# Optimization experiments

Hardware: AMD Instinct MI355X
Metric: run time of the kernel (lower is better)

## Reference

```python
import jax, jax.numpy as jnp
import numpy as np

N = 100_000    # nodes
E = 3_200_000  # distance-labeled multi-hop edges (self-loops excluded upstream)
F = 128        # num_features
H = 128        # hidden (emb_sizes all 128)
C = 40         # num_classes
K = 5          # max_distance
BN_EPS = 1e-5
GIN_EPS = 0.0  # eps=0, learnable_eps=False


def _bn(h, g, b):
    # BatchNorm1d in training mode: biased batch stats over the node axis
    m = h.mean(axis=0)
    v = jnp.mean((h - m) ** 2, axis=0)
    return g * (h - m) * jax.lax.rsqrt(v + BN_EPS) + b


def _spn_layer(h, src, dst, dist, hc, Wa, ba, ga, bta, Wb, bb, gb, btb):
    # SPN layer: softmax per-hop weights, weighted sum aggregation over
    # distance-labeled edges, GIN-style combine, 2-layer MLP (Linear+BN+ReLU).
    w = jax.nn.softmax(hc)                 # [K]
    msg = w[dist][:, None] * h[src]        # [E, H]
    agg = jax.ops.segment_sum(msg, dst, num_segments=N)  # [N, H]
    z = (1.0 + GIN_EPS) * h + agg
    z = jax.nn.relu(_bn(z @ Wa + ba, ga, bta))
    z = jax.nn.relu(_bn(z @ Wb + bb, gb, btb))
    return z


def setup_inputs() -> dict:
    key = jax.random.key(0)
    ks = jax.random.split(key, 16)
    def w(i, shape, s):
        return jax.random.normal(ks[i], shape, dtype=jnp.float32) * s
    sF = 1.0 / np.sqrt(F)
    sH = 1.0 / np.sqrt(H)
    z = lambda n: jnp.zeros((n,), jnp.float32)
    o = lambda n: jnp.ones((n,), jnp.float32)
    return {
        "x": jax.random.normal(ks[0], (N, F), dtype=jnp.float32),
        "edge_index": jax.random.randint(ks[1], (2, E), 0, N, dtype=jnp.int32),
        "edge_dist": jax.random.randint(ks[2], (E,), 0, K, dtype=jnp.int32),  # hop idx = distance-1
        "Wi": w(3, (F, H), sF), "bi": z(H), "gi": o(H), "bti": z(H),
        "hc0": w(4, (K,), 1.0),
        "W0a": w(5, (H, H), sH), "b0a": z(H), "g0a": o(H), "bt0a": z(H),
        "W0b": w(6, (H, H), sH), "b0b": z(H), "g0b": o(H), "bt0b": z(H),
        "hc1": w(7, (K,), 1.0),
        "W1a": w(8, (H, H), sH), "b1a": z(H), "g1a": o(H), "bt1a": z(H),
        "W1b": w(9, (H, H), sH), "b1b": z(H), "g1b": o(H), "bt1b": z(H),
        "Wp1": w(10, (H, H), sH), "bp1": z(H), "gp1": o(H), "btp1": z(H),
        "Wp2": w(11, (H, C), sH), "bp2": z(C),
    }


def reference(x, edge_index, edge_dist, Wi, bi, gi, bti,
              hc0, W0a, b0a, g0a, bt0a, W0b, b0b, g0b, bt0b,
              hc1, W1a, b1a, g1a, bt1a, W1b, b1b, g1b, bt1b,
              Wp1, bp1, gp1, btp1, Wp2, bp2):
    src, dst = edge_index[0], edge_index[1]
    # initial MLP (size=1, final_activation=True)
    h = jax.nn.relu(_bn(x @ Wi + bi, gi, bti))
    # two SPN message-passing layers (dropout is identity at inference)
    h = _spn_layer(h, src, dst, edge_dist, hc0, W0a, b0a, g0a, bt0a, W0b, b0b, g0b, bt0b)
    h = _spn_layer(h, src, dst, edge_dist, hc1, W1a, b1a, g1a, bt1a, W1b, b1b, g1b, bt1b)
    # prediction head (size=2, final_activation=False)
    h = jax.nn.relu(_bn(h @ Wp1 + bp1, gp1, btp1))
    return h @ Wp2 + bp2
```

## Files before the change

kernel.cpp:

```cpp
#include <hip/hip_runtime.h>

#define NN 100000
#define EE 3200000
#define HH 128
#define CC 40
#define KK 5
#define NBUK 391
#define CH 8192
#define CH2 16384

typedef __attribute__((ext_vector_type(8))) short bf16x8;
typedef __attribute__((ext_vector_type(4))) float f32x4;

__device__ inline float b2f(unsigned short u) {
    union { unsigned int i; float f; } c;
    c.i = ((unsigned int)u) << 16;
    return c.f;
}
__device__ inline float b2f_lo(unsigned int u) {
    union { unsigned int i; float f; } c;
    c.i = u << 16;
    return c.f;
}
__device__ inline float b2f_hi(unsigned int u) {
    union { unsigned int i; float f; } c;
    c.i = u & 0xFFFF0000u;
    return c.f;
}
__device__ inline unsigned short f2b(float f) {
    union { float f; unsigned int i; } c;
    c.f = f;
    unsigned int r = c.i + 0x7FFFu + ((c.i >> 16) & 1u);
    return (unsigned short)(r >> 16);
}

__global__ __launch_bounds__(512) void bucket_hist_kernel(const int* __restrict__ dst,
                                                          int* __restrict__ bdeg) {
    __shared__ int h[512];
    int t = threadIdx.x;
    h[t] = 0;
    __syncthreads();
    int base = blockIdx.x * CH2;
    int end = base + CH2;
    if (end > EE) end = EE;
    for (int e = base + t; e < end; e += 512) atomicAdd(&h[dst[e] >> 8], 1);
    __syncthreads();
    int v = h[t];
    if (v > 0) atomicAdd(&bdeg[t], v);
}

__global__ void bucket_scan_kernel(const int* __restrict__ bdeg, int* __restrict__ bbase,
                                   int* __restrict__ gcur, int* __restrict__ offsets,
                                   const float* __restrict__ hc0, const float* __restrict__ hc1,
                                   float* __restrict__ wsm) {
    __shared__ int sh[512];
    int t = threadIdx.x;
    int v = (t < NBUK) ? bdeg[t] : 0;
    sh[t] = v;
    __syncthreads();
    for (int off = 1; off < 512; off <<= 1) {
        int x = (t >= off) ? sh[t - off] : 0;
        __syncthreads();
        sh[t] += x;
        __syncthreads();
    }
    if (t < NBUK) {
        int b = sh[t] - v;
        bbase[t] = b;
        gcur[t] = b;
    }
    if (t == 0) {
        bbase[NBUK] = EE;
        offsets[NN] = EE;
        for (int which = 0; which < 2; ++which) {
            const float* hc = which ? hc1 : hc0;
            float mx = hc[0];
            for (int k = 1; k < KK; ++k) mx = fmaxf(mx, hc[k]);
            float ex0 = expf(hc[0] - mx), ex1 = expf(hc[1] - mx), ex2 = expf(hc[2] - mx);
            float ex3 = expf(hc[3] - mx), ex4 = expf(hc[4] - mx);
            float inv = 1.0f / (ex0 + ex1 + ex2 + ex3 + ex4);
            wsm[which * 8 + 0] = ex0 * inv;
            wsm[which * 8 + 1] = ex1 * inv;
            wsm[which * 8 + 2] = ex2 * inv;
            wsm[which * 8 + 3] = ex3 * inv;
            wsm[which * 8 + 4] = ex4 * inv;
        }
    }
}

__global__ __launch_bounds__(512) void coarse_scatter_kernel(const int* __restrict__ src,
                                                             const int* __restrict__ dst,
                                                             const int* __restrict__ dist,
                                                             int* __restrict__ gcur,
                                                             int* __restrict__ coarse) {
    __shared__ int cnt[512];
    __shared__ int scn[512];
    __shared__ int lofs[512];
    __shared__ int gb[512];
    __shared__ int staging[CH];
    __shared__ int tgt[CH];
    int t = threadIdx.x;
    int base = blockIdx.x * CH;

    cnt[t] = 0;
    __syncthreads();

    int val[16], bb[16];
#pragma unroll
    for (int jj = 0; jj < 16; ++jj) {
        int e = base + jj * 512 + t;
        if (e < EE) {
            int d = dst[e];
            int b = d >> 8;
            bb[jj] = b;
            val[jj] = src[e] | (dist[e] << 17) | ((d & 255) << 20);
            atomicAdd(&cnt[b], 1);
        } else {
            bb[jj] = -1;
            val[jj] = 0;
        }
    }
    __syncthreads();

    int c = cnt[t];
    scn[t] = c;
    __syncthreads();
    for (int off = 1; off < 512; off <<= 1) {
        int x = (t >= off) ? scn[t - off] : 0;
        __syncthreads();
        scn[t] += x;
        __syncthreads();
    }
    lofs[t] = scn[t] - c;
    if (t < NBUK && c > 0) gb[t] = atomicAdd(&gcur[t], c);
    cnt[t] = 0;
    __syncthreads();

#pragma unroll
    for (int jj = 0; jj < 16; ++jj) {
        int b = bb[jj];
        if (b >= 0) {
            int pos = atomicAdd(&cnt[b], 1);
            int slot = lofs[b] + pos;
            staging[slot] = val[jj];
            tgt[slot] = gb[b] + pos;
        }
    }
    __syncthreads();

    int total = scn[511];
    for (int j = t; j < total; j += 512) coarse[tgt[j]] = staging[j];
}

__global__ __launch_bounds__(512) void fine_scatter_kernel(const int* __restrict__ coarse,
                                                           const int* __restrict__ bbase,
                                                           int* __restrict__ offsets,
                                                           int* __restrict__ sorted) {
    __shared__ int cnt[256];
    __shared__ int scn[256];
    __shared__ int cur[256];
    int b = blockIdx.x;
    int t = threadIdx.x;
    if (t < 256) cnt[t] = 0;
    __syncthreads();
    int sb = bbase[b], se = bbase[b + 1];
    for (int idx = sb + t; idx < se; idx += 512)
        atomicAdd(&cnt[(coarse[idx] >> 20) & 255], 1);
    __syncthreads();
    int c = (t < 256) ? cnt[t] : 0;
    if (t < 256) scn[t] = c;
    __syncthreads();
    for (int off = 1; off < 256; off <<= 1) {
        int x = 0;
        if (t < 256 && t >= off) x = scn[t - off];
        __syncthreads();
        if (t < 256) scn[t] += x;
        __syncthreads();
    }
    if (t < 256) {
        int pos = sb + scn[t] - c;
        int node = (b << 8) + t;
        if (node < NN) offsets[node] = pos;
        cur[t] = pos;
    }
    __syncthreads();
    for (int idx = sb + t; idx < se; idx += 512) {
        int v = coarse[idx];
        int p = atomicAdd(&cur[(v >> 20) & 255], 1);
        sorted[p] = (v & 0x1FFFF) | (((v >> 17) & 7) << 20);
    }
}


__global__ __launch_bounds__(256) void convert_x_kernel(const float* __restrict__ x,
                                                        unsigned short* __restrict__ xb) {
    size_t i = (size_t)(blockIdx.x * 256 + threadIdx.x) * 4;
    float4 v = *(const float4*)(x + i);
    ushort4 o;
    o.x = f2b(v.x);
    o.y = f2b(v.y);
    o.z = f2b(v.z);
    o.w = f2b(v.w);
    *(ushort4*)(xb + i) = o;
}

__global__ __launch_bounds__(256) void prep_w_kernel(const float* W0, const float* W1,
                                                     const float* W2, const float* W3,
                                                     const float* W4, const float* W5,
                                                     const float* W6,
                                                     unsigned short* __restrict__ dst) {
    int idx = blockIdx.x * 256 + threadIdx.x;
    if (idx >= 7 * 16384) return;
    int wi = idx / 16384, r = idx - wi * 16384;
    int n = r & 127, k = r >> 7;
    const float* W = wi == 0 ? W0 : wi == 1 ? W1 : wi == 2 ? W2 : wi == 3 ? W3
                   : wi == 4 ? W4 : wi == 5 ? W5 : W6;
    int ncol = (wi == 6) ? CC : 128;
    float v = (n < ncol) ? W[k * ncol + n] : 0.f;
    dst[wi * 16384 + n * 128 + k] = f2b(v);
}


template <int NT, bool TRANSFORM, bool STATS, bool OUTF32>
__global__ __launch_bounds__(256) void mfma_gemm(const unsigned short* __restrict__ Zin,
                                                 const unsigned short* __restrict__ Wt,
                                                 const float* __restrict__ bias, int ncol_real,
                                                 const float* __restrict__ ab,
                                                 void* __restrict__ Uout,
                                                 float* __restrict__ stats) {
    __shared__ unsigned short Zs[128 * 128];
    __shared__ unsigned short Ws[NT * 16 * 128];
    int t = threadIdx.x;
    int m0 = blockIdx.x * 128;
    int c8 = t & 15;

    float av[8], dv[8];
    if constexpr (TRANSFORM) {
#pragma unroll
        for (int j = 0; j < 8; ++j) {
            av[j] = ab[c8 * 8 + j];
            dv[j] = ab[128 + c8 * 8 + j];
        }
    }
#pragma unroll
    for (int it = 0; it < 8; ++it) {
        int chunk = it * 256 + t;
        int r = chunk >> 4;
        int gr = m0 + r;
        bf16x8 v = {};
        if (gr < NN) v = *(const bf16x8*)(Zin + (size_t)gr * 128 + c8 * 8);
        if constexpr (TRANSFORM) {
#pragma unroll
            for (int j = 0; j < 8; ++j) {
                float f = fmaxf(0.f, fmaf(av[j], b2f((unsigned short)v[j]), dv[j]));
                v[j] = (short)f2b(f);
            }
        }
        int ks = c8 * 8;
        *(bf16x8*)(&Zs[r * 128 + (ks ^ ((r & 7) << 3))]) = v;
    }
    for (int chunk = t; chunk < NT * 16 * 16; chunk += 256) {
        int r = chunk >> 4, cc = chunk & 15;
        bf16x8 v = *(const bf16x8*)(Wt + r * 128 + cc * 8);
        int ks = cc * 8;
        *(bf16x8*)(&Ws[r * 128 + (ks ^ ((r & 7) << 3))]) = v;
    }
    __syncthreads();

    int l = t & 63, w = t >> 6;
    int lr = l & 15, lg = l >> 4;

    f32x4 acc[2][NT];
#pragma unroll
    for (int mt = 0; mt < 2; ++mt)
#pragma unroll
        for (int nt = 0; nt < NT; ++nt) acc[mt][nt] = (f32x4){0.f, 0.f, 0.f, 0.f};

#pragma unroll
    for (int kc = 0; kc < 4; ++kc) {
        int ks = kc * 32 + lg * 8;
        bf16x8 afr[2];
#pragma unroll
        for (int mt = 0; mt < 2; ++mt) {
            int row = w * 32 + mt * 16 + lr;
            afr[mt] = *(const bf16x8*)(&Zs[row * 128 + (ks ^ ((row & 7) << 3))]);
        }
#pragma unroll
        for (int nt = 0; nt < NT; ++nt) {
            int n = nt * 16 + lr;
            bf16x8 bfr = *(const bf16x8*)(&Ws[n * 128 + (ks ^ ((n & 7) << 3))]);
            acc[0][nt] = __builtin_amdgcn_mfma_f32_16x16x32_bf16(afr[0], bfr, acc[0][nt], 0, 0, 0);
            acc[1][nt] = __builtin_amdgcn_mfma_f32_16x16x32_bf16(afr[1], bfr, acc[1][nt], 0, 0, 0);
        }
    }

    float bv[NT];
#pragma unroll
    for (int nt = 0; nt < NT; ++nt) {
        int col = nt * 16 + lr;
        bv[nt] = (col < ncol_real) ? bias[col] : 0.f;
    }
    float s1[NT], s2[NT];
    if constexpr (STATS) {
#pragma unroll
        for (int nt = 0; nt < NT; ++nt) { s1[nt] = 0.f; s2[nt] = 0.f; }
    }

#pragma unroll
    for (int mt = 0; mt < 2; ++mt) {
#pragma unroll
        for (int j = 0; j < 4; ++j) {
            int row = m0 + w * 32 + mt * 16 + lg * 4 + j;
            bool rv = row < NN;
#pragma unroll
            for (int nt = 0; nt < NT; ++nt) {
                float val = acc[mt][nt][j] + bv[nt];
                int col = nt * 16 + lr;
                if constexpr (STATS) {
                    if (rv) { s1[nt] += val; s2[nt] += val * val; }
                }
                if (rv && col < ncol_real) {
                    if constexpr (OUTF32)
                        ((float*)Uout)[(size_t)row * ncol_real + col] = val;
                    else
                        ((unsigned short*)Uout)[(size_t)row * 128 + col] = f2b(val);
                }
            }
        }
    }

    if constexpr (STATS) {
        float* slot = stats + (blockIdx.x & 31) * 256;
#pragma unroll
        for (int nt = 0; nt < NT; ++nt) {
            float a = s1[nt], b = s2[nt];
            a += __shfl_xor(a, 16, 64);
            b += __shfl_xor(b, 16, 64);
            a += __shfl_xor(a, 32, 64);
            b += __shfl_xor(b, 32, 64);
            if (lg == 0) {
                atomicAdd(slot + nt * 16 + lr, a);
                atomicAdd(slot + 128 + nt * 16 + lr, b);
            }
        }
    }
}

__global__ void bn_finalize_kernel(const float* __restrict__ stats, const float* __restrict__ g,
                                   const float* __restrict__ beta, float* __restrict__ ab) {
    int ci = threadIdx.x;
    float s = 0.f, s2 = 0.f;
    for (int k = 0; k < 32; ++k) {
        s += stats[k * 256 + ci];
        s2 += stats[k * 256 + 128 + ci];
    }
    float m = s * (1.0f / NN);
    float var = s2 * (1.0f / NN) - m * m;
    float a = g[ci] * rsqrtf(var + 1e-5f);
    ab[ci] = a;
    ab[128 + ci] = beta[ci] - a * m;
}

__global__ __launch_bounds__(128) void agg_kernel(const unsigned short* __restrict__ U,
                                                  const int* __restrict__ offsets,
                                                  const int* __restrict__ sorted,
                                                  const float* __restrict__ ab,
                                                  const float* __restrict__ wsm,
                                                  unsigned short* __restrict__ Z) {
    __shared__ int ebuf[128];
    __shared__ float wl[8];
    __shared__ f32x4 red[4][32];
    int i = blockIdx.x;
    int t = threadIdx.x;
    int grp = t >> 5;
    int sl = t & 31;
    if (t < KK) wl[t] = wsm[t];

    float a0 = ab[sl * 4 + 0], a1 = ab[sl * 4 + 1], a2 = ab[sl * 4 + 2], a3 = ab[sl * 4 + 3];
    float d0 = ab[128 + sl * 4 + 0], d1 = ab[128 + sl * 4 + 1];
    float d2 = ab[128 + sl * 4 + 2], d3 = ab[128 + sl * 4 + 3];

    int beg = offsets[i], end = offsets[i + 1];
    float acc0 = 0.f, acc1 = 0.f, acc2 = 0.f, acc3 = 0.f;

    for (int base = beg; base < end; base += 128) {
        int n = end - base;
        if (n > 128) n = 128;
        __syncthreads();
        if (t < n) ebuf[t] = sorted[base + t];
        __syncthreads();
        int nfull = n & ~31;
        for (int j0 = grp * 8; j0 < nfull; j0 += 32) {
            uint2 uu[8];
            float ww[8];
#pragma unroll
            for (int k = 0; k < 8; ++k) {
                int e = ebuf[j0 + k];
                ww[k] = wl[e >> 20];
                uu[k] = *(const uint2*)((const char*)U +
                                        ((unsigned int)(e & 0xFFFFF) << 8) + (sl << 3));
            }
#pragma unroll
            for (int k = 0; k < 8; ++k) {
                acc0 = fmaf(ww[k], fmaxf(0.f, fmaf(a0, b2f_lo(uu[k].x), d0)), acc0);
                acc1 = fmaf(ww[k], fmaxf(0.f, fmaf(a1, b2f_hi(uu[k].x), d1)), acc1);
                acc2 = fmaf(ww[k], fmaxf(0.f, fmaf(a2, b2f_lo(uu[k].y), d2)), acc2);
                acc3 = fmaf(ww[k], fmaxf(0.f, fmaf(a3, b2f_hi(uu[k].y), d3)), acc3);
            }
        }
        for (int j = nfull + grp; j < n; j += 4) {
            int e = ebuf[j];
            unsigned int sidx = (unsigned int)(e & 0xFFFFF);
            float w = wl[e >> 20];
            uint2 u = *(const uint2*)((const char*)U + (sidx << 8) + (sl << 3));
            acc0 = fmaf(w, fmaxf(0.f, fmaf(a0, b2f_lo(u.x), d0)), acc0);
            acc1 = fmaf(w, fmaxf(0.f, fmaf(a1, b2f_hi(u.x), d1)), acc1);
            acc2 = fmaf(w, fmaxf(0.f, fmaf(a2, b2f_lo(u.y), d2)), acc2);
            acc3 = fmaf(w, fmaxf(0.f, fmaf(a3, b2f_hi(u.y), d3)), acc3);
        }
    }
    red[grp][sl] = (f32x4){acc0, acc1, acc2, acc3};
    __syncthreads();

    if (t < 64) {
        const float* rf = (const float*)red;
        int c0 = t * 2, c1 = t * 2 + 1;
        float s0 = rf[c0] + rf[128 + c0] + rf[256 + c0] + rf[384 + c0];
        float s1 = rf[c1] + rf[128 + c1] + rf[256 + c1] + rf[384 + c1];
        unsigned int ui = *(const unsigned int*)((const char*)U + ((unsigned int)i << 8) + (t << 2));
        float sa0 = ab[c0], sa1 = ab[c1], sd0 = ab[128 + c0], sd1 = ab[128 + c1];
        s0 += fmaxf(0.f, fmaf(sa0, b2f_lo(ui), sd0));
        s1 += fmaxf(0.f, fmaf(sa1, b2f_hi(ui), sd1));
        unsigned int o = (unsigned int)f2b(s0) | ((unsigned int)f2b(s1) << 16);
        *(unsigned int*)((char*)Z + ((unsigned int)i << 8) + (t << 2)) = o;
    }
}


extern "C" void kernel_launch(void* const* d_in, const int* in_sizes, int n_in,
                              void* d_out, int out_size, void* d_ws, size_t ws_size,
                              hipStream_t stream) {
    const float* x = (const float*)d_in[0];
    const int* ei = (const int*)d_in[1];
    const int* ed = (const int*)d_in[2];
    const float* Wi = (const float*)d_in[3];
    const float* bi = (const float*)d_in[4];
    const float* gi = (const float*)d_in[5];
    const float* bti = (const float*)d_in[6];
    const float* hc0 = (const float*)d_in[7];
    const float* W0a = (const float*)d_in[8];
    const float* b0a = (const float*)d_in[9];
    const float* g0a = (const float*)d_in[10];
    const float* bt0a = (const float*)d_in[11];
    const float* W0b = (const float*)d_in[12];
    const float* b0b = (const float*)d_in[13];
    const float* g0b = (const float*)d_in[14];
    const float* bt0b = (const float*)d_in[15];
    const float* hc1 = (const float*)d_in[16];
    const float* W1a = (const float*)d_in[17];
    const float* b1a = (const float*)d_in[18];
    const float* g1a = (const float*)d_in[19];
    const float* bt1a = (const float*)d_in[20];
    const float* W1b = (const float*)d_in[21];
    const float* b1b = (const float*)d_in[22];
    const float* g1b = (const float*)d_in[23];
    const float* bt1b = (const float*)d_in[24];
    const float* Wp1 = (const float*)d_in[25];
    const float* bp1 = (const float*)d_in[26];
    const float* gp1 = (const float*)d_in[27];
    const float* btp1 = (const float*)d_in[28];
    const float* Wp2 = (const float*)d_in[29];
    const float* bp2 = (const float*)d_in[30];
    float* out = (float*)d_out;

    const int* srcv = ei;
    const int* dstv = ei + EE;

    unsigned short* bufX = (unsigned short*)d_ws;
    unsigned short* bufA = bufX + (size_t)NN * HH;
    unsigned short* bufB = bufA + (size_t)NN * HH;
    unsigned short* wt = bufB + (size_t)NN * HH;
    int* sorted = (int*)(wt + 7 * 16384);
    int* coarse = sorted + EE;
    int* offsets = coarse + EE;
    float* stats = (float*)(offsets + NN + 4);
    float* bnab = stats + 6 * 32 * 256;
    float* wsm = bnab + 6 * 256;
    int* gcur = (int*)(wsm + 16);
    int* bdeg = gcur + 512;
    int* bbase = bdeg + 512;

    hipMemsetAsync(stats, 0, (size_t)(6 * 32 * 256) * sizeof(float), stream);
    hipMemsetAsync(bdeg, 0, 512 * sizeof(int), stream);

    bucket_hist_kernel<<<(EE + CH2 - 1) / CH2, 512, 0, stream>>>(dstv, bdeg);
    bucket_scan_kernel<<<1, 512, 0, stream>>>(bdeg, bbase, gcur, offsets, hc0, hc1, wsm);
    coarse_scatter_kernel<<<(EE + CH - 1) / CH, 512, 0, stream>>>(srcv, dstv, ed, gcur, coarse);
    fine_scatter_kernel<<<NBUK, 512, 0, stream>>>(coarse, bbase, offsets, sorted);

    convert_x_kernel<<<(NN * HH / 4 + 255) / 256, 256, 0, stream>>>(x, bufX);
    prep_w_kernel<<<(7 * 16384 + 255) / 256, 256, 0, stream>>>(Wi, W0a, W0b, W1a, W1b, Wp1, Wp2, wt);

    int gg = (NN + 127) / 128;

    mfma_gemm<8, false, true, false><<<gg, 256, 0, stream>>>(bufX, wt, bi, 128, nullptr, bufA, stats);
    bn_finalize_kernel<<<1, 128, 0, stream>>>(stats, gi, bti, bnab);

    agg_kernel<<<NN, 128, 0, stream>>>(bufA, offsets, sorted, bnab, wsm, bufB);
    mfma_gemm<8, false, true, false><<<gg, 256, 0, stream>>>(bufB, wt + 16384, b0a, 128, nullptr,
                                                             bufA, stats + 8192);
    bn_finalize_kernel<<<1, 128, 0, stream>>>(stats + 8192, g0a, bt0a, bnab + 256);
    mfma_gemm<8, true, true, false><<<gg, 256, 0, stream>>>(bufA, wt + 2 * 16384, b0b, 128,
                                                            bnab + 256, bufB, stats + 2 * 8192);
    bn_finalize_kernel<<<1, 128, 0, stream>>>(stats + 2 * 8192, g0b, bt0b, bnab + 512);

    agg_kernel<<<NN, 128, 0, stream>>>(bufB, offsets, sorted, bnab + 512, wsm + 8, bufA);
    mfma_gemm<8, false, true, false><<<gg, 256, 0, stream>>>(bufA, wt + 3 * 16384, b1a, 128,
                                                             nullptr, bufB, stats + 3 * 8192);
    bn_finalize_kernel<<<1, 128, 0, stream>>>(stats + 3 * 8192, g1a, bt1a, bnab + 768);
    mfma_gemm<8, true, true, false><<<gg, 256, 0, stream>>>(bufB, wt + 4 * 16384, b1b, 128,
                                                            bnab + 768, bufA, stats + 4 * 8192);
    bn_finalize_kernel<<<1, 128, 0, stream>>>(stats + 4 * 8192, g1b, bt1b, bnab + 1024);

    mfma_gemm<8, true, true, false><<<gg, 256, 0, stream>>>(bufA, wt + 5 * 16384, bp1, 128,
                                                            bnab + 1024, bufB, stats + 5 * 8192);
    bn_finalize_kernel<<<1, 128, 0, stream>>>(stats + 5 * 8192, gp1, btp1, bnab + 1280);
    mfma_gemm<3, true, false, true><<<gg, 256, 0, stream>>>(bufB, wt + 6 * 16384, bp2, CC,
                                                            bnab + 1280, out, nullptr);

    (void)in_sizes; (void)n_in; (void)out_size; (void)ws_size;
}
```

Measured before the change: 572.1 us.

## Fuse x fp32-to-bf16 conversion into first GEMM and widen aggregation loads

Removes the separate convert_x kernel: the first GEMM now reads the fp32 input directly and converts it to bf16 while staging it in shared memory. The aggregation kernel is restructured so each edge row is gathered by 16 lanes using 16-byte loads (8 edge slots per block instead of 4), with an 8-way shared-memory reduction. The two memsets are merged into one larger memset. This trades fewer kernel launches and less intermediate traffic for more registers per lane in the gather and a larger reduction buffer.

```diff
diff --git a/kernel.cpp b/kernel.cpp
--- a/kernel.cpp
+++ b/kernel.cpp
@@ -192,18 +192,6 @@
 }
 
 
-__global__ __launch_bounds__(256) void convert_x_kernel(const float* __restrict__ x,
-                                                        unsigned short* __restrict__ xb) {
-    size_t i = (size_t)(blockIdx.x * 256 + threadIdx.x) * 4;
-    float4 v = *(const float4*)(x + i);
-    ushort4 o;
-    o.x = f2b(v.x);
-    o.y = f2b(v.y);
-    o.z = f2b(v.z);
-    o.w = f2b(v.w);
-    *(ushort4*)(xb + i) = o;
-}
-
 __global__ __launch_bounds__(256) void prep_w_kernel(const float* W0, const float* W1,
                                                      const float* W2, const float* W3,
                                                      const float* W4, const float* W5,
@@ -221,8 +209,8 @@
 }
 
 
-template <int NT, bool TRANSFORM, bool STATS, bool OUTF32>
-__global__ __launch_bounds__(256) void mfma_gemm(const unsigned short* __restrict__ Zin,
+template <int NT, bool TRANSFORM, bool STATS, bool OUTF32, bool CVTIN>
+__global__ __launch_bounds__(256) void mfma_gemm(const void* __restrict__ ZinV,
                                                  const unsigned short* __restrict__ Wt,
                                                  const float* __restrict__ bias, int ncol_real,
                                                  const float* __restrict__ ab,
@@ -248,12 +236,25 @@
         int r = chunk >> 4;
         int gr = m0 + r;
         bf16x8 v = {};
-        if (gr < NN) v = *(const bf16x8*)(Zin + (size_t)gr * 128 + c8 * 8);
-        if constexpr (TRANSFORM) {
-#pragma unroll
-            for (int j = 0; j < 8; ++j) {
-                float f = fmaxf(0.f, fmaf(av[j], b2f((unsigned short)v[j]), dv[j]));
-                v[j] = (short)f2b(f);
+        if constexpr (CVTIN) {
+            const float* Zf = (const float*)ZinV;
+            if (gr < NN) {
+                float4 f0 = *(const float4*)(Zf + (size_t)gr * 128 + c8 * 8);
+                float4 f1 = *(const float4*)(Zf + (size_t)gr * 128 + c8 * 8 + 4);
+                v[0] = (short)f2b(f0.x); v[1] = (short)f2b(f0.y);
+                v[2] = (short)f2b(f0.z); v[3] = (short)f2b(f0.w);
+                v[4] = (short)f2b(f1.x); v[5] = (short)f2b(f1.y);
+                v[6] = (short)f2b(f1.z); v[7] = (short)f2b(f1.w);
+            }
+        } else {
+            const unsigned short* Zin = (const unsigned short*)ZinV;
+            if (gr < NN) v = *(const bf16x8*)(Zin + (size_t)gr * 128 + c8 * 8);
+            if constexpr (TRANSFORM) {
+#pragma unroll
+                for (int j = 0; j < 8; ++j) {
+                    float f = fmaxf(0.f, fmaf(av[j], b2f((unsigned short)v[j]), dv[j]));
+                    v[j] = (short)f2b(f);
+                }
             }
         }
         int ks = c8 * 8;
@@ -369,19 +370,22 @@
                                                   unsigned short* __restrict__ Z) {
     __shared__ int ebuf[128];
     __shared__ float wl[8];
-    __shared__ f32x4 red[4][32];
+    __shared__ float red[8][128];
     int i = blockIdx.x;
     int t = threadIdx.x;
-    int grp = t >> 5;
-    int sl = t & 31;
+    int slot = t >> 4;
+    int sl = t & 15;
     if (t < KK) wl[t] = wsm[t];
 
-    float a0 = ab[sl * 4 + 0], a1 = ab[sl * 4 + 1], a2 = ab[sl * 4 + 2], a3 = ab[sl * 4 + 3];
-    float d0 = ab[128 + sl * 4 + 0], d1 = ab[128 + sl * 4 + 1];
-    float d2 = ab[128 + sl * 4 + 2], d3 = ab[128 + sl * 4 + 3];
+    float av[8], dv[8];
+#pragma unroll
+    for (int j = 0; j < 8; ++j) {
+        av[j] = ab[sl * 8 + j];
+        dv[j] = ab[128 + sl * 8 + j];
+    }
 
     int beg = offsets[i], end = offsets[i + 1];
-    float acc0 = 0.f, acc1 = 0.f, acc2 = 0.f, acc3 = 0.f;
+    float acc[8] = {};
 
     for (int base = beg; base < end; base += 128) {
         int n = end - base;
@@ -390,49 +394,56 @@
         if (t < n) ebuf[t] = sorted[base + t];
         __syncthreads();
         int nfull = n & ~31;
-        for (int j0 = grp * 8; j0 < nfull; j0 += 32) {
-            uint2 uu[8];
-            float ww[8];
-#pragma unroll
-            for (int k = 0; k < 8; ++k) {
+        for (int j0 = slot * 4; j0 < nfull; j0 += 32) {
+            uint4 uu[4];
+            float ww[4];
+#pragma unroll
+            for (int k = 0; k < 4; ++k) {
                 int e = ebuf[j0 + k];
                 ww[k] = wl[e >> 20];
-                uu[k] = *(const uint2*)((const char*)U +
-                                        ((unsigned int)(e & 0xFFFFF) << 8) + (sl << 3));
+                uu[k] = *(const uint4*)((const char*)U +
+                                        ((unsigned int)(e & 0xFFFFF) << 8) + (sl << 4));
             }
 #pragma unroll
-            for (int k = 0; k < 8; ++k) {
-                acc0 = fmaf(ww[k], fmaxf(0.f, fmaf(a0, b2f_lo(uu[k].x), d0)), acc0);
-                acc1 = fmaf(ww[k], fmaxf(0.f, fmaf(a1, b2f_hi(uu[k].x), d1)), acc1);
-                acc2 = fmaf(ww[k], fmaxf(0.f, fmaf(a2, b2f_lo(uu[k].y), d2)), acc2);
-                acc3 = fmaf(ww[k], fmaxf(0.f, fmaf(a3, b2f_hi(uu[k].y), d3)), acc3);
+            for (int k = 0; k < 4; ++k) {
+                acc[0] = fmaf(ww[k], fmaxf(0.f, fmaf(av[0], b2f_lo(uu[k].x), dv[0])), acc[0]);
+                acc[1] = fmaf(ww[k], fmaxf(0.f, fmaf(av[1], b2f_hi(uu[k].x), dv[1])), acc[1]);
+                acc[2] = fmaf(ww[k], fmaxf(0.f, fmaf(av[2], b2f_lo(uu[k].y), dv[2])), acc[2]);
+                acc[3] = fmaf(ww[k], fmaxf(0.f, fmaf(av[3], b2f_hi(uu[k].y), dv[3])), acc[3]);
+                acc[4] = fmaf(ww[k], fmaxf(0.f, fmaf(av[4], b2f_lo(uu[k].z), dv[4])), acc[4]);
+                acc[5] = fmaf(ww[k], fmaxf(0.f, fmaf(av[5], b2f_hi(uu[k].z), dv[5])), acc[5]);
+                acc[6] = fmaf(ww[k], fmaxf(0.f, fmaf(av[6], b2f_lo(uu[k].w), dv[6])), acc[6]);
+                acc[7] = fmaf(ww[k], fmaxf(0.f, fmaf(av[7], b2f_hi(uu[k].w), dv[7])), acc[7]);
             }
         }
-        for (int j = nfull + grp; j < n; j += 4) {
+        for (int j = nfull + slot; j < n; j += 8) {
             int e = ebuf[j];
-            unsigned int sidx = (unsigned int)(e & 0xFFFFF);
             float w = wl[e >> 20];
-            uint2 u = *(const uint2*)((const char*)U + (sidx << 8) + (sl << 3));
-            acc0 = fmaf(w, fmaxf(0.f, fmaf(a0, b2f_lo(u.x), d0)), acc0);
-            acc1 = fmaf(w, fmaxf(0.f, fmaf(a1, b2f_hi(u.x), d1)), acc1);
-            acc2 = fmaf(w, fmaxf(0.f, fmaf(a2, b2f_lo(u.y), d2)), acc2);
-            acc3 = fmaf(w, fmaxf(0.f, fmaf(a3, b2f_hi(u.y), d3)), acc3);
-        }
-    }
-    red[grp][sl] = (f32x4){acc0, acc1, acc2, acc3};
-    __syncthreads();
-
-    if (t < 64) {
-        const float* rf = (const float*)red;
-        int c0 = t * 2, c1 = t * 2 + 1;
-        float s0 = rf[c0] + rf[128 + c0] + rf[256 + c0] + rf[384 + c0];
-        float s1 = rf[c1] + rf[128 + c1] + rf[256 + c1] + rf[384 + c1];
-        unsigned int ui = *(const unsigned int*)((const char*)U + ((unsigned int)i << 8) + (t << 2));
-        float sa0 = ab[c0], sa1 = ab[c1], sd0 = ab[128 + c0], sd1 = ab[128 + c1];
-        s0 += fmaxf(0.f, fmaf(sa0, b2f_lo(ui), sd0));
-        s1 += fmaxf(0.f, fmaf(sa1, b2f_hi(ui), sd1));
-        unsigned int o = (unsigned int)f2b(s0) | ((unsigned int)f2b(s1) << 16);
-        *(unsigned int*)((char*)Z + ((unsigned int)i << 8) + (t << 2)) = o;
+            uint4 u = *(const uint4*)((const char*)U +
+                                      ((unsigned int)(e & 0xFFFFF) << 8) + (sl << 4));
+            acc[0] = fmaf(w, fmaxf(0.f, fmaf(av[0], b2f_lo(u.x), dv[0])), acc[0]);
+            acc[1] = fmaf(w, fmaxf(0.f, fmaf(av[1], b2f_hi(u.x), dv[1])), acc[1]);
+            acc[2] = fmaf(w, fmaxf(0.f, fmaf(av[2], b2f_lo(u.y), dv[2])), acc[2]);
+            acc[3] = fmaf(w, fmaxf(0.f, fmaf(av[3], b2f_hi(u.y), dv[3])), acc[3]);
+            acc[4] = fmaf(w, fmaxf(0.f, fmaf(av[4], b2f_lo(u.z), dv[4])), acc[4]);
+            acc[5] = fmaf(w, fmaxf(0.f, fmaf(av[5], b2f_hi(u.z), dv[5])), acc[5]);
+            acc[6] = fmaf(w, fmaxf(0.f, fmaf(av[6], b2f_lo(u.w), dv[6])), acc[6]);
+            acc[7] = fmaf(w, fmaxf(0.f, fmaf(av[7], b2f_hi(u.w), dv[7])), acc[7]);
+        }
+    }
+    *(f32x4*)(&red[slot][sl * 8]) = (f32x4){acc[0], acc[1], acc[2], acc[3]};
+    *(f32x4*)(&red[slot][sl * 8 + 4]) = (f32x4){acc[4], acc[5], acc[6], acc[7]};
+    __syncthreads();
+
+    float s = 0.f;
+#pragma unroll
+    for (int s8 = 0; s8 < 8; ++s8) s += red[s8][t];
+    float u = b2f(U[((size_t)i << 7) + t]);
+    s += fmaxf(0.f, fmaf(ab[t], u, ab[128 + t]));
+    float so = __shfl_xor(s, 1, 64);
+    if ((t & 1) == 0) {
+        unsigned int o = (unsigned int)f2b(s) | ((unsigned int)f2b(so) << 16);
+        *(unsigned int*)((char*)Z + ((unsigned int)i << 8) + (t << 1)) = o;
     }
 }
 
@@ -476,8 +487,7 @@
     const int* srcv = ei;
     const int* dstv = ei + EE;
 
-    unsigned short* bufX = (unsigned short*)d_ws;
-    unsigned short* bufA = bufX + (size_t)NN * HH;
+    unsigned short* bufA = (unsigned short*)d_ws;
     unsigned short* bufB = bufA + (size_t)NN * HH;
     unsigned short* wt = bufB + (size_t)NN * HH;
     int* sorted = (int*)(wt + 7 * 16384);
@@ -490,43 +500,45 @@
     int* bdeg = gcur + 512;
     int* bbase = bdeg + 512;
 
-    hipMemsetAsync(stats, 0, (size_t)(6 * 32 * 256) * sizeof(float), stream);
-    hipMemsetAsync(bdeg, 0, 512 * sizeof(int), stream);
+    hipMemsetAsync(stats, 0, (size_t)(6 * 32 * 256 + 6 * 256 + 16 + 512 + 512) * 4, stream);
 
     bucket_hist_kernel<<<(EE + CH2 - 1) / CH2, 512, 0, stream>>>(dstv, bdeg);
     bucket_scan_kernel<<<1, 512, 0, stream>>>(bdeg, bbase, gcur, offsets, hc0, hc1, wsm);
     coarse_scatter_kernel<<<(EE + CH - 1) / CH, 512, 0, stream>>>(srcv, dstv, ed, gcur, coarse);
     fine_scatter_kernel<<<NBUK, 512, 0, stream>>>(coarse, bbase, offsets, sorted);
 
-    convert_x_kernel<<<(NN * HH / 4 + 255) / 256, 256, 0, stream>>>(x, bufX);
     prep_w_kernel<<<(7 * 16384 + 255) / 256, 256, 0, stream>>>(Wi, W0a, W0b, W1a, W1b, Wp1, Wp2, wt);
 
     int gg = (NN + 127) / 128;
 
-    mfma_gemm<8, false, true, false><<<gg, 256, 0, stream>>>(bufX, wt, bi, 128, nullptr, bufA, stats);
+    mfma_gemm<8, false, true, false, true><<<gg, 256, 0, stream>>>(x, wt, bi, 128, nullptr, bufA,
+                                                                   stats);
     bn_finalize_kernel<<<1, 128, 0, stream>>>(stats, gi, bti, bnab);
 
     agg_kernel<<<NN, 128, 0, stream>>>(bufA, offsets, sorted, bnab, wsm, bufB);
-    mfma_gemm<8, false, true, false><<<gg, 256, 0, stream>>>(bufB, wt + 16384, b0a, 128, nullptr,
-                                                             bufA, stats + 8192);
+    mfma_gemm<8, false, true, false, false><<<gg, 256, 0, stream>>>(bufB, wt + 16384, b0a, 128,
+                                                                    nullptr, bufA, stats + 8192);
     bn_finalize_kernel<<<1, 128, 0, stream>>>(stats + 8192, g0a, bt0a, bnab + 256);
-    mfma_gemm<8, true, true, false><<<gg, 256, 0, stream>>>(bufA, wt + 2 * 16384, b0b, 128,
-                                                            bnab + 256, bufB, stats + 2 * 8192);
+    mfma_gemm<8, true, true, false, false><<<gg, 256, 0, stream>>>(bufA, wt + 2 * 16384, b0b, 128,
+                                                                   bnab + 256, bufB,
+                                                                   stats + 2 * 8192);
     bn_finalize_kernel<<<1, 128, 0, stream>>>(stats + 2 * 8192, g0b, bt0b, bnab + 512);
 
     agg_kernel<<<NN, 128, 0, stream>>>(bufB, offsets, sorted, bnab + 512, wsm + 8, bufA);
-    mfma_gemm<8, false, true, false><<<gg, 256, 0, stream>>>(bufA, wt + 3 * 16384, b1a, 128,
-                                                             nullptr, bufB, stats + 3 * 8192);
+    mfma_gemm<8, false, true, false, false><<<gg, 256, 0, stream>>>(bufA, wt + 3 * 16384, b1a, 128,
+                                                                    nullptr, bufB, stats + 3 * 8192);
     bn_finalize_kernel<<<1, 128, 0, stream>>>(stats + 3 * 8192, g1a, bt1a, bnab + 768);
-    mfma_gemm<8, true, true, false><<<gg, 256, 0, stream>>>(bufB, wt + 4 * 16384, b1b, 128,
-                                                            bnab + 768, bufA, stats + 4 * 8192);
+    mfma_gemm<8, true, true, false, false><<<gg, 256, 0, stream>>>(bufB, wt + 4 * 16384, b1b, 128,
+                                                                   bnab + 768, bufA,
+                                                                   stats + 4 * 8192);
     bn_finalize_kernel<<<1, 128, 0, stream>>>(stats + 4 * 8192, g1b, bt1b, bnab + 1024);
 
-    mfma_gemm<8, true, true, false><<<gg, 256, 0, stream>>>(bufA, wt + 5 * 16384, bp1, 128,
-                                                            bnab + 1024, bufB, stats + 5 * 8192);
+    mfma_gemm<8, true, true, false, false><<<gg, 256, 0, stream>>>(bufA, wt + 5 * 16384, bp1, 128,
+                                                                   bnab + 1024, bufB,
+                                                                   stats + 5 * 8192);
     bn_finalize_kernel<<<1, 128, 0, stream>>>(stats + 5 * 8192, gp1, btp1, bnab + 1280);
-    mfma_gemm<3, true, false, true><<<gg, 256, 0, stream>>>(bufB, wt + 6 * 16384, bp2, CC,
-                                                            bnab + 1280, out, nullptr);
+    mfma_gemm<3, true, false, true, false><<<gg, 256, 0, stream>>>(bufB, wt + 6 * 16384, bp2, CC,
+                                                                   bnab + 1280, out, nullptr);
 
     (void)in_sizes; (void)n_in; (void)out_size; (void)ws_size;
 }
```

Result: faster. 557.7 us, median of 2 (-2.5%).
